# Performance work log

Measured on AMD Instinct MI355X. Metric: run time of the kernel, lower is better.

## Reference

```python
import jax, jax.numpy as jnp
import numpy as np

B, S, HID = 1, 2048, 2048
N_HEADS, N_KV, HD = 32, 8, 64
GROUPS = N_HEADS // N_KV            # repeat_kv factor = 4
WEB_RANGE = 4                        # -> split 16 local-mask heads / 16 web-mask heads
SPLIT2 = int(N_HEADS * (WEB_RANGE / 8.0))  # 16
SPLIT1 = N_HEADS - SPLIT2                  # 16
ROPE_THETA = 10000.0
RMS_EPS = 1e-6
NEG = -1e9


def setup_inputs() -> dict:
    key = jax.random.key(0)
    ks = jax.random.split(key, 8)
    hidden_states = jax.random.normal(ks[0], (B, S, HID), jnp.float32)
    position_ids = jnp.broadcast_to(jnp.arange(S, dtype=jnp.int64), (B, S))
    # causal additive mask [1,1,S,S]
    tril = jnp.tril(jnp.ones((S, S), bool))
    attention_mask = jnp.where(tril, 0.0, NEG)[None, None].astype(jnp.float32)
    # web mask: causal AND random web-structure keep pattern (diag always kept)
    keep = jax.random.bernoulli(ks[1], 0.5, (S, S)) | jnp.eye(S, dtype=bool)
    web_attention_mask = jnp.where(tril & keep, 0.0, NEG)[None, None].astype(jnp.float32)
    sc = 0.02
    Wq = jax.random.normal(ks[2], (HID, N_HEADS * HD), jnp.float32) * sc
    Wk = jax.random.normal(ks[3], (HID, N_KV * HD), jnp.float32) * sc
    Wv = jax.random.normal(ks[4], (HID, N_KV * HD), jnp.float32) * sc
    Wo = jax.random.normal(ks[5], (N_HEADS * HD, HID), jnp.float32) * sc
    q_ln_w = jnp.ones((HD,), jnp.float32)
    k_ln_w = jnp.ones((HD,), jnp.float32)
    return dict(hidden_states=hidden_states, position_ids=position_ids,
                attention_mask=attention_mask, web_attention_mask=web_attention_mask,
                Wq=Wq, Wk=Wk, Wv=Wv, Wo=Wo, q_ln_w=q_ln_w, k_ln_w=k_ln_w)


def _rotate_half(x):
    x1, x2 = jnp.split(x, 2, axis=-1)
    return jnp.concatenate([-x2, x1], axis=-1)


def _rope_cos_sin(position_ids):
    inv_freq = 1.0 / (ROPE_THETA ** (jnp.arange(0, HD, 2, dtype=jnp.float32) / HD))  # [HD/2]
    freqs = position_ids.astype(jnp.float32)[..., None] * inv_freq                   # [B,S,HD/2]
    emb = jnp.concatenate([freqs, freqs], axis=-1)                                   # [B,S,HD]
    return jnp.cos(emb)[:, None], jnp.sin(emb)[:, None]                              # [B,1,S,HD]


def _rmsnorm(x, w):
    var = jnp.mean(x * x, axis=-1, keepdims=True)
    return x * jax.lax.rsqrt(var + RMS_EPS) * w


def _sdpa(q, k, v, mask):
    scale = 1.0 / jnp.sqrt(jnp.float32(HD))
    scores = jnp.einsum('bhqd,bhkd->bhqk', q, k) * scale + mask
    p = jax.nn.softmax(scores, axis=-1)
    return jnp.einsum('bhqk,bhkd->bhqd', p, v)


def reference(hidden_states, position_ids, attention_mask, web_attention_mask,
              Wq, Wk, Wv, Wo, q_ln_w, k_ln_w):
    b, s, _ = hidden_states.shape
    q = (hidden_states @ Wq).reshape(b, s, N_HEADS, HD).transpose(0, 2, 1, 3)  # [B,H,S,D]
    k = (hidden_states @ Wk).reshape(b, s, N_KV, HD).transpose(0, 2, 1, 3)     # [B,KV,S,D]
    v = (hidden_states @ Wv).reshape(b, s, N_KV, HD).transpose(0, 2, 1, 3)
    cos, sin = _rope_cos_sin(position_ids)
    q = q * cos + _rotate_half(q) * sin
    k = k * cos + _rotate_half(k) * sin
    # qk layer norms (applied after RoPE, as in the source)
    q = _rmsnorm(q, q_ln_w)
    k = _rmsnorm(k, k_ln_w)
    # repeat_kv (GQA -> MHA)
    k = jnp.repeat(k, GROUPS, axis=1)
    v = jnp.repeat(v, GROUPS, axis=1)
    # split heads into two groups, each with its own mask
    o1 = _sdpa(q[:, :SPLIT1], k[:, :SPLIT1], v[:, :SPLIT1], attention_mask)
    o2 = _sdpa(q[:, SPLIT1:], k[:, SPLIT1:], v[:, SPLIT1:], web_attention_mask)
    attn = jnp.concatenate([o1, o2], axis=1)                 # [B,H,S,D]
    attn = attn.transpose(0, 2, 1, 3).reshape(b, s, N_HEADS * HD)
    return attn @ Wo
```

## Files before the change

kernel.cpp:

```cpp
#include <hip/hip_runtime.h>
#include <stdint.h>


typedef unsigned short u16;
typedef unsigned short u16x4 __attribute__((ext_vector_type(4)));
typedef unsigned short u16x8 __attribute__((ext_vector_type(8)));
typedef __bf16 bf16x8 __attribute__((ext_vector_type(8)));
typedef float f32x4 __attribute__((ext_vector_type(4)));
typedef float f32x16 __attribute__((ext_vector_type(16)));

#define SLEN 2048
#define HIDDEN 2048
#define QKVN 3072
#define QSCALE 0.18033688011112042f

#define CFENCE() asm volatile("" ::: "memory")

__device__ __forceinline__ u16 f2bf(float x) {
  uint32_t u = __float_as_uint(x);
  return (u16)((u + 0x7FFFu + ((u >> 16) & 1u)) >> 16);
}

__device__ __forceinline__ float bf2f(u16 x) {
  return __uint_as_float((uint32_t)x << 16);
}

__device__ __forceinline__ uint32_t cvtpk_bf16(float lo, float hi) {
  uint32_t r;
  asm("v_cvt_pk_bf16_f32 %0, %1, %2" : "=v"(r) : "v"(lo), "v"(hi));
  return r;
}

__device__ __forceinline__ float fast_exp2(float x) {
  float r;
  asm("v_exp_f32 %0, %1" : "=v"(r) : "v"(x));
  return r;
}

__device__ __forceinline__ float xhalf_sum(float x) {
  auto r = __builtin_amdgcn_permlane32_swap(__float_as_uint(x), __float_as_uint(x),
                                            false, false);
  return __uint_as_float(r[0]) + __uint_as_float(r[1]);
}

__device__ __forceinline__ void gload_lds16(const void* g, void* l) {
  __builtin_amdgcn_global_load_lds(
      (const __attribute__((address_space(1))) void*)g,
      (__attribute__((address_space(3))) void*)l, 16, 0, 0);
}

__device__ __forceinline__ void transpose_tile(const float* in, int ldin,
                                               u16* out, int ldout,
                                               int k0, int n0, int tid,
                                               float (*tile)[33]) {
  int x = tid & 31, y = tid >> 5;
#pragma unroll
  for (int i = 0; i < 32; i += 8)
    tile[y + i][x] = in[(size_t)(k0 + y + i) * ldin + n0 + x];
  __syncthreads();
#pragma unroll
  for (int i = 0; i < 32; i += 8)
    out[(size_t)(n0 + y + i) * ldout + k0 + x] = f2bf(tile[x][y + i]);
}

__global__ __launch_bounds__(256) void prep_all(const float* __restrict__ hidden,
                                                u16* __restrict__ hbf,
                                                const float* __restrict__ Wq,
                                                const float* __restrict__ Wk,
                                                const float* __restrict__ Wv,
                                                const float* __restrict__ Wo,
                                                u16* __restrict__ Wcat,
                                                u16* __restrict__ Wot,
                                                const float* __restrict__ webmask,
                                                uint32_t* __restrict__ mbits) {
  __shared__ float tile[32][33];
  const int b = blockIdx.x, tid = threadIdx.x;
  if (b < 4096) {
    int idx = (b * 256 + tid) * 4;
    float4 v = *(const float4*)(hidden + idx);
    u16x4 o;
    o[0] = f2bf(v.x); o[1] = f2bf(v.y); o[2] = f2bf(v.z); o[3] = f2bf(v.w);
    *(u16x4*)(hbf + idx) = o;
  } else if (b < 8192) {
    int t = b - 4096;
    transpose_tile(Wq, 2048, Wcat, 2048, (t & 63) * 32, (t >> 6) * 32, tid, tile);
  } else if (b < 9216) {
    int t = b - 8192;
    transpose_tile(Wk, 512, Wcat + (size_t)2048 * 2048, 2048,
                   (t & 63) * 32, (t >> 6) * 32, tid, tile);
  } else if (b < 10240) {
    int t = b - 9216;
    transpose_tile(Wv, 512, Wcat + (size_t)2560 * 2048, 2048,
                   (t & 63) * 32, (t >> 6) * 32, tid, tile);
  } else if (b < 14336) {
    int t = b - 10240;
    transpose_tile(Wo, 2048, Wot, 2048, (t & 63) * 32, (t >> 6) * 32, tid, tile);
  } else {
    int w = (b - 14336) * 256 + tid;
    const float* p = webmask + (size_t)w * 32;
    uint32_t bits = 0;
#pragma unroll
    for (int j = 0; j < 32; ++j) bits |= (p[j] > -0.5f ? 1u : 0u) << j;
    mbits[(size_t)(w & 63) * 2048 + (w >> 6)] = bits;
  }
}

template <int WN, int OUTBF>
__global__ __launch_bounds__(256) void gemm_tn(const u16* __restrict__ A,
                                               const u16* __restrict__ B,
                                               void* __restrict__ Cv,
                                               int N, int K) {
  constexpr int BN = WN * 32;
  __shared__ u16 As[2][128 * 64];
  __shared__ u16 Bs[2][BN * 64];
  const int tid = threadIdx.x;
  const int w = tid >> 6, l = tid & 63;
  const int lin = blockIdx.x;
  const int xcd = lin & 7, pos = lin >> 3;
  const int bm = ((xcd & 1) << 3) + (pos & 7);
  const int bn = ((xcd >> 1) << 2) + (pos >> 3);
  const int wr = w >> 1, wc = w & 1;

  f32x4 acc[4][WN] = {};

  int rowA[4], colA[4], ldsA[4];
#pragma unroll
  for (int g = 0; g < 4; ++g) {
    int c = g * 256 + w * 64 + l;
    rowA[g] = ((c >> 7) << 4) + ((c >> 3) & 15);
    colA[g] = ((c & 7) ^ ((c >> 3) & 7)) * 8;
    ldsA[g] = (g * 256 + w * 64) * 8;
  }
  int rowB[WN], colB[WN], ldsB[WN];
#pragma unroll
  for (int g = 0; g < WN; ++g) {
    int c = g * 256 + w * 64 + l;
    rowB[g] = ((c >> 7) << 4) + ((c >> 3) & 15);
    colB[g] = ((c & 7) ^ ((c >> 3) & 7)) * 8;
    ldsB[g] = (g * 256 + w * 64) * 8;
  }
  const u16* Arow = A + (size_t)(bm * 128) * K;
  const u16* Brow = B + (size_t)(bn * BN) * K;

  auto stage = [&](int buf, int k0) {
#pragma unroll
    for (int g = 0; g < 4; ++g)
      gload_lds16(Arow + (size_t)rowA[g] * K + k0 + colA[g], &As[buf][ldsA[g]]);
#pragma unroll
    for (int g = 0; g < WN; ++g)
      gload_lds16(Brow + (size_t)rowB[g] * K + k0 + colB[g], &Bs[buf][ldsB[g]]);
  };

  const int nk = K >> 6;
  stage(0, 0);

  for (int k = 0; k < nk; ++k) {
    CFENCE(); __builtin_amdgcn_s_barrier(); CFENCE();
    if (k + 1 < nk) {
      stage((k + 1) & 1, (k + 1) * 64);
      if constexpr (WN == 6) asm volatile("s_waitcnt vmcnt(10)" ::: "memory");
      else                   asm volatile("s_waitcnt vmcnt(8)" ::: "memory");
    } else {
      asm volatile("s_waitcnt vmcnt(0)" ::: "memory");
    }
    CFENCE(); __builtin_amdgcn_s_barrier(); CFENCE();
    const int cur = k & 1;
#pragma unroll
    for (int ks = 0; ks < 2; ++ks) {
      const int xq = ((ks * 4 + (l >> 4)) ^ (l & 7)) * 8;
      const int rbase = (l & 15) * 64 + xq;
      bf16x8 af[4], bfr[WN];
#pragma unroll
      for (int mi = 0; mi < 4; ++mi)
        af[mi] = *(const bf16x8*)&As[cur][(wr * 4 + mi) * 1024 + rbase];
#pragma unroll
      for (int ni = 0; ni < WN; ++ni)
        bfr[ni] = *(const bf16x8*)&Bs[cur][(wc * WN + ni) * 1024 + rbase];
#pragma unroll
      for (int mi = 0; mi < 4; ++mi)
#pragma unroll
        for (int ni = 0; ni < WN; ++ni)
          acc[mi][ni] = __builtin_amdgcn_mfma_f32_16x16x32_bf16(af[mi], bfr[ni],
                                                                acc[mi][ni], 0, 0, 0);
    }
  }
  const int cr = (l >> 4) * 4, cc = l & 15;
#pragma unroll
  for (int mi = 0; mi < 4; ++mi) {
    int row0 = bm * 128 + wr * 64 + mi * 16 + cr;
#pragma unroll
    for (int ni = 0; ni < WN; ++ni) {
      int col = bn * BN + wc * (WN * 16) + ni * 16 + cc;
      if constexpr (OUTBF) {
        u16* C = (u16*)Cv;
#pragma unroll
        for (int i = 0; i < 4; ++i)
          C[(size_t)(row0 + i) * N + col] = f2bf(acc[mi][ni][i]);
      } else {
        float* C = (float*)Cv;
#pragma unroll
        for (int i = 0; i < 4; ++i)
          C[(size_t)(row0 + i) * N + col] = acc[mi][ni][i];
      }
    }
  }
}

__global__ __launch_bounds__(256) void rope_vtrans(const u16* __restrict__ qkv,
                                                   const float* __restrict__ qw,
                                                   const float* __restrict__ kw,
                                                   u16* __restrict__ Qo,
                                                   u16* __restrict__ Ko,
                                                   u16* __restrict__ Vt) {
  __shared__ float tile[32][65];
  const int b = blockIdx.x, tid = threadIdx.x;
  if (b < 20480) {
    int s = (b & 511) * 4 + (tid >> 6);
    int hh = b >> 9;
    int d = tid & 63;
    bool isq = hh < 32;
    int col = isq ? hh * 64 + d : 2048 + (hh - 32) * 64 + d;
    float x = bf2f(qkv[(size_t)s * QKVN + col]);
    int i = d & 31;
    float inv_freq = exp2f(-(float)i * (13.287712379549449f / 32.0f));
    float ang = (float)s * inv_freq;
    float sn, cs;
    __sincosf(ang, &sn, &cs);
    float partner = __shfl_xor(x, 32, 64);
    float y = (d < 32) ? (x * cs - partner * sn) : (x * cs + partner * sn);
    float ss = y * y;
#pragma unroll
    for (int off = 32; off; off >>= 1) ss += __shfl_xor(ss, off, 64);
    float r = rsqrtf(ss * (1.0f / 64.0f) + 1e-6f);
    float o = y * r * (isq ? qw[d] : kw[d]);
    if (isq) Qo[((size_t)hh * SLEN + s) * 64 + d] = f2bf(o * QSCALE);
    else     Ko[((size_t)(hh - 32) * SLEN + s) * 64 + d] = f2bf(o);
  } else {
    int t = b - 20480;
    int kv = t >> 6;
    int s0 = (t & 63) * 32;
    int d = tid & 63, r4 = tid >> 6;
#pragma unroll
    for (int i = 0; i < 32; i += 4)
      tile[i + r4][d] = bf2f(qkv[(size_t)(s0 + i + r4) * QKVN + 2560 + kv * 64 + d]);
    __syncthreads();
    int dr = tid >> 2, sc = (tid & 3) * 8;
    u16x8 o;
#pragma unroll
    for (int j = 0; j < 8; ++j) o[j] = f2bf(tile[sc + j][dr]);
    *(u16x8*)(Vt + (((size_t)kv * 64 + (s0 >> 5)) * 64 + dr) * 32 + sc) = o;
  }
}

__global__ __launch_bounds__(256) void attn_fused(const u16* __restrict__ Q,
                                                  const u16* __restrict__ Kh,
                                                  const u16* __restrict__ Vt,
                                                  const uint32_t* __restrict__ mbits,
                                                  u16* __restrict__ Aout) {
  __shared__ float accS[4 * 32 * 64];
  __shared__ float lS[4 * 32];
  const int w = threadIdx.x >> 6, l = threadIdx.x & 63;
  const int lin = blockIdx.x;
  const int xcd = lin & 7, pos = lin >> 3;
  const int h = xcd * 4 + (pos & 3);
  const int j = pos >> 2;
  const int hkv = h >> 2;
  const bool web = (h >= 16);
  const int l31 = l & 31, hi = l >> 5;
  const int qrel = l31 - 4 * hi;

  const u16* Kp = Kh + ((size_t)hkv * SLEN + l31) * 64 + hi * 8;
  const u16* Vbase = Vt + (size_t)hkv * 64 * SLEN;
  const int voff = l31 * 32 + hi * 8;

#define LOADSET(P, kbn)                                                         \
  do {                                                                          \
    const u16* knp_ = Kp + (size_t)(kbn) * 2048;                                \
    P##k0 = *(const bf16x8*)(knp_);                                             \
    P##k1 = *(const bf16x8*)(knp_ + 16);                                        \
    P##k2 = *(const bf16x8*)(knp_ + 32);                                        \
    P##k3 = *(const bf16x8*)(knp_ + 48);                                        \
    const u16* vnp_ = Vbase + (size_t)(kbn) * 2048 + voff;                      \
    P##v0 = *(const bf16x8*)(vnp_);                                             \
    P##v1 = *(const bf16x8*)(vnp_ + 16);                                        \
    P##v2 = *(const bf16x8*)(vnp_ + 1024);                                      \
    P##v3 = *(const bf16x8*)(vnp_ + 1024 + 16);                                 \
    if (web) P##m = mrowT[(size_t)(kbn) * 2048];                                \
  } while (0)

#define COMPUTE(P, kbv)                                                         \
  do {                                                                          \
    const int kb_ = (kbv);                                                      \
    __builtin_amdgcn_s_setprio(1);                                              \
    f32x16 s = {};                                                              \
    s = __builtin_amdgcn_mfma_f32_32x32x16_bf16(P##k0, qf0, s, 0, 0, 0);        \
    s = __builtin_amdgcn_mfma_f32_32x32x16_bf16(P##k1, qf1, s, 0, 0, 0);        \
    s = __builtin_amdgcn_mfma_f32_32x32x16_bf16(P##k2, qf2, s, 0, 0, 0);        \
    s = __builtin_amdgcn_mfma_f32_32x32x16_bf16(P##k3, qf3, s, 0, 0, 0);        \
    __builtin_amdgcn_s_setprio(0);                                              \
    if (web) {                                                                  \
      uint32_t word = P##m >> (hi * 4);                                         \
      if (kb_ == qt) {                                                          \
        _Pragma("unroll")                                                       \
        for (int r = 0; r < 16; ++r) {                                          \
          const int ki = (r & 3) + 8 * (r >> 2);                                \
          bool keep = ((word >> ki) & 1u) && (ki <= qrel);                      \
          s[r] = keep ? s[r] : -1e9f;                                           \
        }                                                                       \
      } else {                                                                  \
        _Pragma("unroll")                                                       \
        for (int r = 0; r < 16; ++r) {                                          \
          const int ki = (r & 3) + 8 * (r >> 2);                                \
          s[r] = ((word >> ki) & 1u) ? s[r] : -1e9f;                            \
        }                                                                       \
      }                                                                         \
    } else if (kb_ == qt) {                                                     \
      _Pragma("unroll")                                                         \
      for (int r = 0; r < 16; ++r) {                                            \
        const int ki = (r & 3) + 8 * (r >> 2);                                  \
        s[r] = (ki <= qrel) ? s[r] : -1e9f;                                     \
      }                                                                         \
    }                                                                           \
    f32x16 p;                                                                   \
    _Pragma("unroll")                                                           \
    for (int r = 0; r < 16; ++r) p[r] = fast_exp2(s[r]);                        \
    float rs = ((p[0] + p[1]) + (p[2] + p[3])) + ((p[4] + p[5]) + (p[6] + p[7]))\
             + ((p[8] + p[9]) + (p[10] + p[11]))                                \
             + ((p[12] + p[13]) + (p[14] + p[15]));                             \
    llh += rs;                                                                  \
    uint32_t a0 = cvtpk_bf16(p[0], p[1]),   b0 = cvtpk_bf16(p[2], p[3]);        \
    uint32_t c0 = cvtpk_bf16(p[4], p[5]),   d0 = cvtpk_bf16(p[6], p[7]);        \
    uint32_t a1 = cvtpk_bf16(p[8], p[9]),   b1 = cvtpk_bf16(p[10], p[11]);      \
    uint32_t c1 = cvtpk_bf16(p[12], p[13]), d1 = cvtpk_bf16(p[14], p[15]);      \
    auto r0 = __builtin_amdgcn_permlane32_swap(a0, c0, false, false);           \
    auto r1 = __builtin_amdgcn_permlane32_swap(b0, d0, false, false);           \
    auto r2 = __builtin_amdgcn_permlane32_swap(a1, c1, false, false);           \
    auto r3 = __builtin_amdgcn_permlane32_swap(b1, d1, false, false);           \
    union { uint32_t wv[4]; bf16x8 v; } pf0u, pf1u;                             \
    pf0u.wv[0] = r0[0]; pf0u.wv[1] = r1[0]; pf0u.wv[2] = r0[1]; pf0u.wv[3] = r1[1]; \
    pf1u.wv[0] = r2[0]; pf1u.wv[1] = r3[0]; pf1u.wv[2] = r2[1]; pf1u.wv[3] = r3[1]; \
    __builtin_amdgcn_s_setprio(1);                                              \
    acc0 = __builtin_amdgcn_mfma_f32_32x32x16_bf16(P##v0, pf0u.v, acc0, 0, 0, 0); \
    acc0 = __builtin_amdgcn_mfma_f32_32x32x16_bf16(P##v1, pf1u.v, acc0, 0, 0, 0); \
    acc1 = __builtin_amdgcn_mfma_f32_32x32x16_bf16(P##v2, pf0u.v, acc1, 0, 0, 0); \
    acc1 = __builtin_amdgcn_mfma_f32_32x32x16_bf16(P##v3, pf1u.v, acc1, 0, 0, 0); \
    __builtin_amdgcn_s_setprio(0);                                              \
  } while (0)

#pragma unroll
  for (int t = 0; t < 2; ++t) {
    const int qt = t == 0 ? (63 - j) : j;
    const int q0 = qt * 32;
    const int nkb = qt + 1;
    const uint32_t* mrowT = mbits + q0 + l31;

    const u16* Qp = Q + ((size_t)h * SLEN + q0 + l31) * 64 + hi * 8;
    bf16x8 qf0 = *(const bf16x8*)(Qp);
    bf16x8 qf1 = *(const bf16x8*)(Qp + 16);
    bf16x8 qf2 = *(const bf16x8*)(Qp + 32);
    bf16x8 qf3 = *(const bf16x8*)(Qp + 48);

    f32x16 acc0 = {}, acc1 = {};
    float llh = 0.f;

    if (w < nkb) {
      bf16x8 Ak0, Ak1, Ak2, Ak3, Av0, Av1, Av2, Av3;
      bf16x8 Bk0, Bk1, Bk2, Bk3, Bv0, Bv1, Bv2, Bv3;
      uint32_t Am = 0, Bm = 0;
      int kb = w;
      LOADSET(A, kb);
      while (true) {
        if (kb + 4 < nkb) LOADSET(B, kb + 4);
        COMPUTE(A, kb);
        kb += 4;
        if (kb >= nkb) break;
        if (kb + 4 < nkb) LOADSET(A, kb + 4);
        COMPUTE(B, kb);
        kb += 4;
        if (kb >= nkb) break;
      }
    }
    const float ll = xhalf_sum(llh);
    if (hi == 0) lS[w * 32 + l31] = ll;
    float* wbase = accS + w * 2048 + (l31 << 6);
    const int sw = (l31 & 15) << 2;
#pragma unroll
    for (int tt = 0; tt < 4; ++tt) {
      int dA = (8 * tt + 4 * hi) ^ sw;
      int dB = (32 + 8 * tt + 4 * hi) ^ sw;
      float4 v0 = {acc0[4 * tt], acc0[4 * tt + 1], acc0[4 * tt + 2], acc0[4 * tt + 3]};
      float4 v1 = {acc1[4 * tt], acc1[4 * tt + 1], acc1[4 * tt + 2], acc1[4 * tt + 3]};
      *(float4*)(wbase + dA) = v0;
      *(float4*)(wbase + dB) = v1;
    }
    __syncthreads();
    const int q = threadIdx.x & 31;
    const int dd = (threadIdx.x >> 5) * 8;
    float L = (lS[q] + lS[32 + q]) + (lS[64 + q] + lS[96 + q]);
    const int offA = (q << 6) + (dd ^ ((q & 15) << 2));
    const int offB = offA ^ 4;
    float o[8];
    {
      float4 xa = *(float4*)(accS + offA);
      float4 xb = *(float4*)(accS + offB);
      o[0] = xa.x; o[1] = xa.y; o[2] = xa.z; o[3] = xa.w;
      o[4] = xb.x; o[5] = xb.y; o[6] = xb.z; o[7] = xb.w;
    }
#pragma unroll
    for (int ww = 1; ww < 4; ++ww) {
      float4 xa = *(float4*)(accS + ww * 2048 + offA);
      float4 xb = *(float4*)(accS + ww * 2048 + offB);
      o[0] += xa.x; o[1] += xa.y; o[2] += xa.z; o[3] += xa.w;
      o[4] += xb.x; o[5] += xb.y; o[6] += xb.z; o[7] += xb.w;
    }
    const float invL = 1.0f / L;
    uint4 pk;
    pk.x = cvtpk_bf16(o[0] * invL, o[1] * invL);
    pk.y = cvtpk_bf16(o[2] * invL, o[3] * invL);
    pk.z = cvtpk_bf16(o[4] * invL, o[5] * invL);
    pk.w = cvtpk_bf16(o[6] * invL, o[7] * invL);
    *(uint4*)(Aout + (size_t)(q0 + q) * HIDDEN + h * 64 + dd) = pk;
    __syncthreads();
  }
#undef LOADSET
#undef COMPUTE
}


extern "C" void kernel_launch(void* const* d_in, const int* in_sizes, int n_in,
                              void* d_out, int out_size, void* d_ws, size_t ws_size,
                              hipStream_t stream) {
  const float* hidden  = (const float*)d_in[0];
  const float* webmask = (const float*)d_in[3];
  const float* Wq = (const float*)d_in[4];
  const float* Wk = (const float*)d_in[5];
  const float* Wv = (const float*)d_in[6];
  const float* Wo = (const float*)d_in[7];
  const float* qlnw = (const float*)d_in[8];
  const float* klnw = (const float*)d_in[9];
  float* out = (float*)d_out;

  char* ws = (char*)d_ws;
  u16*      hbf  = (u16*)(ws);
  u16*      Wcat = (u16*)(ws + (8u << 20));
  u16*      Wot  = (u16*)(ws + (20u << 20));
  u16*      qkv  = (u16*)(ws + (28u << 20));
  u16*      Qh   = (u16*)(ws + (52u << 20));
  u16*      Kh   = (u16*)(ws + (60u << 20));
  u16*      Vt   = (u16*)(ws + (62u << 20));
  u16*      Ao   = (u16*)(ws + (64u << 20));
  uint32_t* mb   = (uint32_t*)(ws + (72u << 20));

  prep_all<<<14848, 256, 0, stream>>>(hidden, hbf, Wq, Wk, Wv, Wo, Wcat, Wot,
                                      webmask, mb);
  gemm_tn<6, 1><<<256, 256, 0, stream>>>(hbf, Wcat, qkv, QKVN, HIDDEN);
  rope_vtrans<<<20992, 256, 0, stream>>>(qkv, qlnw, klnw, Qh, Kh, Vt);
  attn_fused<<<1024, 256, 0, stream>>>(Qh, Kh, Vt, mb, Ao);
  gemm_tn<4, 0><<<256, 256, 0, stream>>>(Ao, Wot, out, HIDDEN, HIDDEN);
}
```

Baseline: 181.9 us.

## Launch one attention block per query tile and store partials in bf16 LDS

The attention kernel previously paired a long and a short causal query tile per block (1024 blocks, two passes). It now launches 2048 blocks, each handling one query tile, with heaviest tiles scheduled first via qt = 63 - pos/4. The cross-wave partial-accumulator buffer in LDS is stored as bf16 instead of fp32, halving shared memory, which may allow more resident blocks. The bf16 partials add rounding error before the cross-wave sum, and the hardware scheduler must now do the load balancing that the tile pairing used to provide.

```diff
diff --git a/kernel.cpp b/kernel.cpp
--- a/kernel.cpp
+++ b/kernel.cpp
@@ -257,13 +257,15 @@
                                                   const u16* __restrict__ Vt,
                                                   const uint32_t* __restrict__ mbits,
                                                   u16* __restrict__ Aout) {
-  __shared__ float accS[4 * 32 * 64];
+  __shared__ u16 accS[4 * 32 * 64];
   __shared__ float lS[4 * 32];
   const int w = threadIdx.x >> 6, l = threadIdx.x & 63;
   const int lin = blockIdx.x;
   const int xcd = lin & 7, pos = lin >> 3;
   const int h = xcd * 4 + (pos & 3);
-  const int j = pos >> 2;
+  const int qt = 63 - (pos >> 2);
+  const int q0 = qt * 32;
+  const int nkb = qt + 1;
   const int hkv = h >> 2;
   const bool web = (h >= 16);
   const int l31 = l & 31, hi = l >> 5;
@@ -272,6 +274,16 @@
   const u16* Kp = Kh + ((size_t)hkv * SLEN + l31) * 64 + hi * 8;
   const u16* Vbase = Vt + (size_t)hkv * 64 * SLEN;
   const int voff = l31 * 32 + hi * 8;
+  const uint32_t* mrowT = mbits + q0 + l31;
+
+  const u16* Qp = Q + ((size_t)h * SLEN + q0 + l31) * 64 + hi * 8;
+  bf16x8 qf0 = *(const bf16x8*)(Qp);
+  bf16x8 qf1 = *(const bf16x8*)(Qp + 16);
+  bf16x8 qf2 = *(const bf16x8*)(Qp + 32);
+  bf16x8 qf3 = *(const bf16x8*)(Qp + 48);
+
+  f32x16 acc0 = {}, acc1 = {};
+  float llh = 0.f;
 
 #define LOADSET(P, kbn)                                                         \
   do {                                                                          \
@@ -347,83 +359,66 @@
     __builtin_amdgcn_s_setprio(0);                                              \
   } while (0)
 
-#pragma unroll
-  for (int t = 0; t < 2; ++t) {
-    const int qt = t == 0 ? (63 - j) : j;
-    const int q0 = qt * 32;
-    const int nkb = qt + 1;
-    const uint32_t* mrowT = mbits + q0 + l31;
-
-    const u16* Qp = Q + ((size_t)h * SLEN + q0 + l31) * 64 + hi * 8;
-    bf16x8 qf0 = *(const bf16x8*)(Qp);
-    bf16x8 qf1 = *(const bf16x8*)(Qp + 16);
-    bf16x8 qf2 = *(const bf16x8*)(Qp + 32);
-    bf16x8 qf3 = *(const bf16x8*)(Qp + 48);
-
-    f32x16 acc0 = {}, acc1 = {};
-    float llh = 0.f;
-
-    if (w < nkb) {
-      bf16x8 Ak0, Ak1, Ak2, Ak3, Av0, Av1, Av2, Av3;
-      bf16x8 Bk0, Bk1, Bk2, Bk3, Bv0, Bv1, Bv2, Bv3;
-      uint32_t Am = 0, Bm = 0;
-      int kb = w;
-      LOADSET(A, kb);
-      while (true) {
-        if (kb + 4 < nkb) LOADSET(B, kb + 4);
-        COMPUTE(A, kb);
-        kb += 4;
-        if (kb >= nkb) break;
-        if (kb + 4 < nkb) LOADSET(A, kb + 4);
-        COMPUTE(B, kb);
-        kb += 4;
-        if (kb >= nkb) break;
-      }
+  if (w < nkb) {
+    bf16x8 Ak0, Ak1, Ak2, Ak3, Av0, Av1, Av2, Av3;
+    bf16x8 Bk0, Bk1, Bk2, Bk3, Bv0, Bv1, Bv2, Bv3;
+    uint32_t Am = 0, Bm = 0;
+    int kb = w;
+    LOADSET(A, kb);
+    while (true) {
+      if (kb + 4 < nkb) LOADSET(B, kb + 4);
+      COMPUTE(A, kb);
+      kb += 4;
+      if (kb >= nkb) break;
+      if (kb + 4 < nkb) LOADSET(A, kb + 4);
+      COMPUTE(B, kb);
+      kb += 4;
+      if (kb >= nkb) break;
     }
-    const float ll = xhalf_sum(llh);
-    if (hi == 0) lS[w * 32 + l31] = ll;
-    float* wbase = accS + w * 2048 + (l31 << 6);
-    const int sw = (l31 & 15) << 2;
-#pragma unroll
-    for (int tt = 0; tt < 4; ++tt) {
-      int dA = (8 * tt + 4 * hi) ^ sw;
-      int dB = (32 + 8 * tt + 4 * hi) ^ sw;
-      float4 v0 = {acc0[4 * tt], acc0[4 * tt + 1], acc0[4 * tt + 2], acc0[4 * tt + 3]};
-      float4 v1 = {acc1[4 * tt], acc1[4 * tt + 1], acc1[4 * tt + 2], acc1[4 * tt + 3]};
-      *(float4*)(wbase + dA) = v0;
-      *(float4*)(wbase + dB) = v1;
-    }
-    __syncthreads();
-    const int q = threadIdx.x & 31;
-    const int dd = (threadIdx.x >> 5) * 8;
-    float L = (lS[q] + lS[32 + q]) + (lS[64 + q] + lS[96 + q]);
-    const int offA = (q << 6) + (dd ^ ((q & 15) << 2));
-    const int offB = offA ^ 4;
-    float o[8];
-    {
-      float4 xa = *(float4*)(accS + offA);
-      float4 xb = *(float4*)(accS + offB);
-      o[0] = xa.x; o[1] = xa.y; o[2] = xa.z; o[3] = xa.w;
-      o[4] = xb.x; o[5] = xb.y; o[6] = xb.z; o[7] = xb.w;
-    }
-#pragma unroll
-    for (int ww = 1; ww < 4; ++ww) {
-      float4 xa = *(float4*)(accS + ww * 2048 + offA);
-      float4 xb = *(float4*)(accS + ww * 2048 + offB);
-      o[0] += xa.x; o[1] += xa.y; o[2] += xa.z; o[3] += xa.w;
-      o[4] += xb.x; o[5] += xb.y; o[6] += xb.z; o[7] += xb.w;
-    }
-    const float invL = 1.0f / L;
-    uint4 pk;
-    pk.x = cvtpk_bf16(o[0] * invL, o[1] * invL);
-    pk.y = cvtpk_bf16(o[2] * invL, o[3] * invL);
-    pk.z = cvtpk_bf16(o[4] * invL, o[5] * invL);
-    pk.w = cvtpk_bf16(o[6] * invL, o[7] * invL);
-    *(uint4*)(Aout + (size_t)(q0 + q) * HIDDEN + h * 64 + dd) = pk;
-    __syncthreads();
   }
 #undef LOADSET
 #undef COMPUTE
+
+  const float ll = xhalf_sum(llh);
+  if (hi == 0) lS[w * 32 + l31] = ll;
+  u16* wbase = accS + w * 2048 + (l31 << 6);
+  const int sw = (l31 & 15) << 2;
+#pragma unroll
+  for (int tt = 0; tt < 4; ++tt) {
+    int dA = (8 * tt + 4 * hi) ^ sw;
+    int dB = (32 + 8 * tt + 4 * hi) ^ sw;
+    uint2 pA, pB;
+    pA.x = cvtpk_bf16(acc0[4 * tt], acc0[4 * tt + 1]);
+    pA.y = cvtpk_bf16(acc0[4 * tt + 2], acc0[4 * tt + 3]);
+    pB.x = cvtpk_bf16(acc1[4 * tt], acc1[4 * tt + 1]);
+    pB.y = cvtpk_bf16(acc1[4 * tt + 2], acc1[4 * tt + 3]);
+    *(uint2*)(wbase + dA) = pA;
+    *(uint2*)(wbase + dB) = pB;
+  }
+  __syncthreads();
+  const int q = threadIdx.x & 31;
+  const int dd = (threadIdx.x >> 5) * 8;
+  float L = (lS[q] + lS[32 + q]) + (lS[64 + q] + lS[96 + q]);
+  const int offA = (q << 6) + (dd ^ ((q & 15) << 2));
+  const int offB = offA ^ 4;
+  float o[8] = {};
+#pragma unroll
+  for (int ww = 0; ww < 4; ++ww) {
+    const u16* pbase = accS + ww * 2048;
+    uint2 xa = *(const uint2*)(pbase + offA);
+    uint2 xb = *(const uint2*)(pbase + offB);
+    o[0] += bf2f((u16)(xa.x & 0xffffu)); o[1] += bf2f((u16)(xa.x >> 16));
+    o[2] += bf2f((u16)(xa.y & 0xffffu)); o[3] += bf2f((u16)(xa.y >> 16));
+    o[4] += bf2f((u16)(xb.x & 0xffffu)); o[5] += bf2f((u16)(xb.x >> 16));
+    o[6] += bf2f((u16)(xb.y & 0xffffu)); o[7] += bf2f((u16)(xb.y >> 16));
+  }
+  const float invL = 1.0f / L;
+  uint4 pk;
+  pk.x = cvtpk_bf16(o[0] * invL, o[1] * invL);
+  pk.y = cvtpk_bf16(o[2] * invL, o[3] * invL);
+  pk.z = cvtpk_bf16(o[4] * invL, o[5] * invL);
+  pk.w = cvtpk_bf16(o[6] * invL, o[7] * invL);
+  *(uint4*)(Aout + (size_t)(q0 + q) * HIDDEN + h * 64 + dd) = pk;
 }
 
 
@@ -455,6 +450,6 @@
                                       webmask, mb);
   gemm_tn<6, 1><<<256, 256, 0, stream>>>(hbf, Wcat, qkv, QKVN, HIDDEN);
   rope_vtrans<<<20992, 256, 0, stream>>>(qkv, qlnw, klnw, Qh, Kh, Vt);
-  attn_fused<<<1024, 256, 0, stream>>>(Qh, Kh, Vt, mb, Ao);
+  attn_fused<<<2048, 256, 0, stream>>>(Qh, Kh, Vt, mb, Ao);
   gemm_tn<4, 0><<<256, 256, 0, stream>>>(Ao, Wot, out, HIDDEN, HIDDEN);
 }
```

New measurement: 184.1 us. No clear change (+1.2%).
